# Performance work log

Hardware: AMD Instinct MI355X
Metric: run time of the kernel (lower is better)

Reference implementation:

```python
import jax, jax.numpy as jnp
import numpy as np

EMB = 384
H = 6
D = 64  # head_size = EMB // H
FF = 4 * EMB
B, T = 256, 256
EPS = 1e-5


def layernorm(x, g, b):
    mu = jnp.mean(x, axis=-1, keepdims=True)
    var = jnp.var(x, axis=-1, keepdims=True)
    return (x - mu) * jax.lax.rsqrt(var + EPS) * g + b


def setup_inputs() -> dict:
    key = jax.random.key(0)
    ks = jax.random.split(key, 12)
    s_qkv = 1.0 / np.sqrt(EMB)
    return {
        "x":  jax.random.normal(ks[0], (B, T, EMB), jnp.float32),
        # per-head Q/K/V projections stacked: [EMB, H, D]
        "Wq": jax.random.normal(ks[1], (EMB, H, D), jnp.float32) * s_qkv,
        "Wk": jax.random.normal(ks[2], (EMB, H, D), jnp.float32) * s_qkv,
        "Wv": jax.random.normal(ks[3], (EMB, H, D), jnp.float32) * s_qkv,
        "Wo": jax.random.normal(ks[4], (EMB, EMB), jnp.float32) * s_qkv,
        "bo": jnp.zeros((EMB,), jnp.float32),
        "W1": jax.random.normal(ks[5], (EMB, FF), jnp.float32) * s_qkv,
        "b1": jnp.zeros((FF,), jnp.float32),
        "W2": jax.random.normal(ks[6], (FF, EMB), jnp.float32) * (1.0 / np.sqrt(FF)),
        "b2": jnp.zeros((EMB,), jnp.float32),
        "g1": jnp.ones((EMB,), jnp.float32),
        "be1": jnp.zeros((EMB,), jnp.float32),
        "g2": jnp.ones((EMB,), jnp.float32),
        "be2": jnp.zeros((EMB,), jnp.float32),
    }


def reference(x, Wq, Wk, Wv, Wo, bo, W1, b1, W2, b2, g1, be1, g2, be2):
    # pre-LN attention (unmasked encoder block, dropout in eval mode = identity)
    h = layernorm(x, g1, be1)                      # [B,T,C]
    q = jnp.einsum('btc,chd->bhtd', h, Wq)
    k = jnp.einsum('btc,chd->bhtd', h, Wk)
    v = jnp.einsum('btc,chd->bhtd', h, Wv)
    scores = jnp.einsum('bhtd,bhsd->bhts', q, k) * (D ** -0.5)
    attn = jax.nn.softmax(scores, axis=-1)         # [B,H,T,T]
    o = jnp.einsum('bhts,bhsd->bhtd', attn, v)
    o = o.transpose(0, 2, 1, 3).reshape(x.shape[0], x.shape[1], EMB)  # concat heads
    x = x + o @ Wo + bo
    h2 = layernorm(x, g2, be2)
    ff = jax.nn.relu(h2 @ W1 + b1) @ W2 + b2
    return x + ff
```

## Files before the change

### kernel.cpp

```cpp
#include <hip/hip_runtime.h>

typedef __attribute__((ext_vector_type(8))) short bf16x8;
typedef __attribute__((ext_vector_type(4))) float f32x4;
typedef __attribute__((ext_vector_type(4))) unsigned short u16x4;
typedef __attribute__((ext_vector_type(4))) unsigned int u32x4;

#define DEVFN static __device__ __forceinline__

DEVFN unsigned short f2b(float f) {
  union { float f; unsigned u; } x; x.f = f;
  unsigned r = x.u + 0x7FFFu + ((x.u >> 16) & 1u);
  return (unsigned short)(r >> 16);
}

DEVFN unsigned cvtpk(float lo, float hi) {
  unsigned r;
  asm("v_cvt_pk_bf16_f32 %0, %1, %2" : "=v"(r) : "v"(lo), "v"(hi));
  return r;
}

DEVFN void gll16(const void* g, void* l) {
  __builtin_amdgcn_global_load_lds(
      (const __attribute__((address_space(1))) unsigned int*)g,
      (__attribute__((address_space(3))) unsigned int*)l, 16, 0, 0);
}

#define MFMA16(a, b, c) __builtin_amdgcn_mfma_f32_16x16x32_bf16((a), (b), (c), 0, 0, 0)

__global__ __launch_bounds__(256) void prep_kernel(
    const float* __restrict__ Wq, const float* __restrict__ Wk, const float* __restrict__ Wv,
    const float* __restrict__ Wo, const float* __restrict__ W1, const float* __restrict__ W2,
    short* __restrict__ wqkvT, short* __restrict__ woT,
    short* __restrict__ w1T, short* __restrict__ w2T)
{
  int idx = blockIdx.x * 256 + threadIdx.x;
  if (idx < 442368) {
    int n = idx / 384, kk = idx - n * 384;
    int sec = n / 384, ww = n - sec * 384;
    const float* s = sec == 0 ? Wq : (sec == 1 ? Wk : Wv);
    wqkvT[idx] = (short)f2b(s[kk * 384 + ww]);
  } else if (idx < 589824) {
    int j = idx - 442368;
    int n = j / 384, kk = j - n * 384;
    woT[j] = (short)f2b(Wo[kk * 384 + n]);
  } else if (idx < 1179648) {
    int j = idx - 589824;
    int n = j / 384, kk = j - n * 384;
    w1T[j] = (short)f2b(W1[kk * 1536 + n]);
  } else if (idx < 1769472) {
    int j = idx - 1179648;
    int n = j / 1536, kk = j - n * 1536;
    w2T[j] = (short)f2b(W2[kk * 384 + n]);
  }
}

__global__ __launch_bounds__(256) void ln_kernel(
    const float* __restrict__ x, const float* __restrict__ g, const float* __restrict__ b,
    short* __restrict__ out)
{
  int row = blockIdx.x * 4 + (threadIdx.x >> 6);
  int l = threadIdx.x & 63;
  const float* xr = x + (size_t)row * 384;
  float v[6], s = 0.f, s2 = 0.f;
  #pragma unroll
  for (int i = 0; i < 6; ++i) { v[i] = xr[l + 64 * i]; s += v[i]; s2 += v[i] * v[i]; }
  #pragma unroll
  for (int m = 1; m < 64; m <<= 1) { s += __shfl_xor(s, m); s2 += __shfl_xor(s2, m); }
  float mu = s * (1.f / 384.f);
  float rs = rsqrtf(s2 * (1.f / 384.f) - mu * mu + 1e-5f);
  short* orow = out + (size_t)row * 384;
  #pragma unroll
  for (int i = 0; i < 6; ++i) {
    int c = l + 64 * i;
    orow[c] = (short)f2b((v[i] - mu) * rs * g[c] + b[c]);
  }
}

template<int EPI>
__global__ __launch_bounds__(512) void gemm_bt(
    const short* __restrict__ A, const short* __restrict__ BT,
    int K, int kt, int N, int nx,
    const float* __restrict__ bias, const float* __restrict__ resid,
    float* __restrict__ fout, short* __restrict__ bout,
    short* __restrict__ qb, short* __restrict__ kb, short* __restrict__ vb)
{
  __shared__ short As[256 * 64];
  __shared__ short Bs[128 * 64];
  const int tid = threadIdx.x;
  const int l = tid & 63, w = tid >> 6;
  const int cl = l & 15, rq = l >> 4;
  const int wr = (w >> 1) * 64, wc = (w & 1) * 64;

  const int nwg = gridDim.x, bid = blockIdx.x;
  const int q8 = nwg >> 3, r8 = nwg & 7;
  const int xcd = bid & 7, ii = bid >> 3;
  const int wg = (xcd < r8) ? xcd * (q8 + 1) + ii : r8 * (q8 + 1) + (xcd - r8) * q8 + ii;
  const int bx = wg % nx, by = wg / nx;

  const int m0 = by * 256, n0 = bx * 128;
  const short* Ab = A + (size_t)m0 * K;
  const short* Bb = BT + (size_t)n0 * K;

  f32x4 acc[4][4] = {};

  for (int ks = 0; ks < kt; ++ks) {
    const int k0 = ks * 64;
    __syncthreads();
    #pragma unroll
    for (int i = 0; i < 4; ++i) {
      int slot = i * 512 + tid;
      int row = slot >> 3, g = slot & 7;
      int gs = g ^ (row & 7);
      gll16(Ab + (size_t)row * K + k0 + gs * 8, &As[slot * 8]);
    }
    #pragma unroll
    for (int i = 0; i < 2; ++i) {
      int slot = i * 512 + tid;
      int row = slot >> 3, g = slot & 7;
      int gs = g ^ (row & 7);
      gll16(Bb + (size_t)row * K + k0 + gs * 8, &Bs[slot * 8]);
    }
    __syncthreads();
    #pragma unroll
    for (int kk = 0; kk < 2; ++kk) {
      bf16x8 af[4], bfr[4];
      #pragma unroll
      for (int m = 0; m < 4; ++m) {
        int row = wr + m * 16 + cl;
        af[m] = *(const bf16x8*)&As[row * 64 + (((kk * 4 + rq) ^ (row & 7)) * 8)];
      }
      #pragma unroll
      for (int n = 0; n < 4; ++n) {
        int row = wc + n * 16 + cl;
        bfr[n] = *(const bf16x8*)&Bs[row * 64 + (((kk * 4 + rq) ^ (row & 7)) * 8)];
      }
      #pragma unroll
      for (int m = 0; m < 4; ++m)
        #pragma unroll
        for (int n = 0; n < 4; ++n)
          acc[m][n] = MFMA16(af[m], bfr[n], acc[m][n]);
    }
  }

  const int gr0 = m0 + wr, gc0 = n0 + wc;
  #pragma unroll
  for (int m = 0; m < 4; ++m) {
    #pragma unroll
    for (int n = 0; n < 4; ++n) {
      int col = gc0 + n * 16 + cl;
      int rbase = gr0 + m * 16 + rq * 4;
      if constexpr (EPI == 0) {
        int sec = col / 384;
        int wcol = col - sec * 384;
        int hh = wcol >> 6, d = wcol & 63;
        int bidx = rbase >> 8, t0 = rbase & 255;
        if (sec == 2) {
          u16x4 pk;
          #pragma unroll
          for (int r = 0; r < 4; ++r) pk[r] = f2b(acc[m][n][r]);
          *(u16x4*)&vb[((size_t)(bidx * 6 + hh) * 64 + d) * 256 + t0] = pk;
        } else {
          short* dst = (sec == 0) ? qb : kb;
          float sc = (sec == 0) ? 0.125f : 1.0f;
          #pragma unroll
          for (int r = 0; r < 4; ++r)
            dst[((size_t)(bidx * 6 + hh) * 256 + t0 + r) * 64 + d] = (short)f2b(acc[m][n][r] * sc);
        }
      } else if constexpr (EPI == 1) {
        #pragma unroll
        for (int r = 0; r < 4; ++r) {
          size_t ix = (size_t)(rbase + r) * N + col;
          fout[ix] = acc[m][n][r] + bias[col] + resid[ix];
        }
      } else {
        #pragma unroll
        for (int r = 0; r < 4; ++r)
          bout[(size_t)(rbase + r) * N + col] = (short)f2b(fmaxf(acc[m][n][r] + bias[col], 0.f));
      }
    }
  }
}

__global__ __launch_bounds__(1024) void attn_kernel(
    const short* __restrict__ qg, const short* __restrict__ kg,
    const short* __restrict__ vg, short* __restrict__ og)
{
  __shared__ short Ks[256 * 64];
  __shared__ short Vs[64 * 256];
  const int tid = threadIdx.x;
  const int bh = blockIdx.x;
  const int w = tid >> 6, l = tid & 63;
  const int cl = l & 15, rq = l >> 4;
  const short* kgb = kg + (size_t)bh * 16384;
  const short* vgb = vg + (size_t)bh * 16384;
  #pragma unroll
  for (int i = 0; i < 2; ++i) {
    int slot = i * 1024 + tid;
    int row = slot >> 3, g = slot & 7;
    gll16(kgb + row * 64 + (g ^ (row & 7)) * 8, &Ks[slot * 8]);
  }
  #pragma unroll
  for (int i = 0; i < 2; ++i) {
    int slot = i * 1024 + tid;
    int row = slot >> 5, g = slot & 31;
    int gs = (g & 24) | ((g ^ row) & 7);
    gll16(vgb + row * 256 + gs * 8, &Vs[slot * 8]);
  }
  const int qrow = w * 16 + cl;
  const bf16x8* qp = (const bf16x8*)(qg + ((size_t)bh * 256 + qrow) * 64 + rq * 8);
  bf16x8 qf0 = qp[0], qf1 = qp[4];
  const int b = bh / 6, hh = bh - b * 6;
  __syncthreads();

  f32x4 s[16] = {};
  #pragma unroll
  for (int c = 0; c < 16; ++c) {
    int srow = c * 16 + cl;
    bf16x8 k0 = *(const bf16x8*)&Ks[srow * 64 + ((rq ^ (srow & 7)) * 8)];
    bf16x8 k1 = *(const bf16x8*)&Ks[srow * 64 + (((4 + rq) ^ (srow & 7)) * 8)];
    s[c] = MFMA16(k0, qf0, s[c]);
    s[c] = MFMA16(k1, qf1, s[c]);
  }
  float mr[8];
  #pragma unroll
  for (int c = 0; c < 8; ++c)
    mr[c] = fmaxf(fmaxf(fmaxf(s[2*c][0], s[2*c][1]), fmaxf(s[2*c][2], s[2*c][3])),
                  fmaxf(fmaxf(s[2*c+1][0], s[2*c+1][1]), fmaxf(s[2*c+1][2], s[2*c+1][3])));
  float m = fmaxf(fmaxf(fmaxf(mr[0], mr[1]), fmaxf(mr[2], mr[3])),
                  fmaxf(fmaxf(mr[4], mr[5]), fmaxf(mr[6], mr[7])));
  m = fmaxf(m, __shfl_xor(m, 16));
  m = fmaxf(m, __shfl_xor(m, 32));
  float tc[16];
  #pragma unroll
  for (int c = 0; c < 16; ++c) {
    #pragma unroll
    for (int r = 0; r < 4; ++r) s[c][r] = __expf(s[c][r] - m);
    tc[c] = (s[c][0] + s[c][1]) + (s[c][2] + s[c][3]);
  }
  float t = ((tc[0]+tc[1])+(tc[2]+tc[3])) + ((tc[4]+tc[5])+(tc[6]+tc[7]))
          + ((tc[8]+tc[9])+(tc[10]+tc[11])) + ((tc[12]+tc[13])+(tc[14]+tc[15]));
  t += __shfl_xor(t, 16);
  t += __shfl_xor(t, 32);
  const float inv = 1.f / t;

  f32x4 oacc[4] = {};
  const int idx1 = (((2 * rq) & 3) * 16 + cl) << 2;
  const int idx2 = (((2 * rq + 1) & 3) * 16 + cl) << 2;
  const bool up = rq >= 2;
  #pragma unroll
  for (int ch = 0; ch < 8; ++ch) {
    int X0 = (int)cvtpk(s[2*ch][0], s[2*ch][1]);
    int X1 = (int)cvtpk(s[2*ch][2], s[2*ch][3]);
    int X2 = (int)cvtpk(s[2*ch+1][0], s[2*ch+1][1]);
    int X3 = (int)cvtpk(s[2*ch+1][2], s[2*ch+1][3]);
    int lo0 = __builtin_amdgcn_ds_bpermute(idx1, X0);
    int lo1 = __builtin_amdgcn_ds_bpermute(idx1, X1);
    int hi0 = __builtin_amdgcn_ds_bpermute(idx1, X2);
    int hi1 = __builtin_amdgcn_ds_bpermute(idx1, X3);
    int lo2 = __builtin_amdgcn_ds_bpermute(idx2, X0);
    int lo3 = __builtin_amdgcn_ds_bpermute(idx2, X1);
    int hi2 = __builtin_amdgcn_ds_bpermute(idx2, X2);
    int hi3 = __builtin_amdgcn_ds_bpermute(idx2, X3);
    u32x4 words;
    words[0] = (unsigned)(up ? hi0 : lo0);
    words[1] = (unsigned)(up ? hi1 : lo1);
    words[2] = (unsigned)(up ? hi2 : lo2);
    words[3] = (unsigned)(up ? hi3 : lo3);
    bf16x8 pa = __builtin_bit_cast(bf16x8, words);
    #pragma unroll
    for (int n = 0; n < 4; ++n) {
      int vrow = n * 16 + cl;
      int gg = ch * 4 + rq;
      int gs = (gg & 24) | ((gg ^ vrow) & 7);
      bf16x8 vf = *(const bf16x8*)&Vs[vrow * 256 + gs * 8];
      oacc[n] = MFMA16(pa, vf, oacc[n]);
    }
  }
  float invr[4];
  #pragma unroll
  for (int r = 0; r < 4; ++r) invr[r] = __shfl(inv, 4 * rq + r);
  #pragma unroll
  for (int n = 0; n < 4; ++n) {
    #pragma unroll
    for (int r = 0; r < 4; ++r) {
      int trow = w * 16 + 4 * rq + r;
      og[((size_t)(b * 256 + trow)) * 384 + hh * 64 + n * 16 + cl] =
          (short)f2b(oacc[n][r] * invr[r]);
    }
  }
}

extern "C" void kernel_launch(void* const* d_in, const int* in_sizes, int n_in,
                              void* d_out, int out_size, void* d_ws, size_t ws_size,
                              hipStream_t stream) {
  const float* x   = (const float*)d_in[0];
  const float* Wq  = (const float*)d_in[1];
  const float* Wk  = (const float*)d_in[2];
  const float* Wv  = (const float*)d_in[3];
  const float* Wo  = (const float*)d_in[4];
  const float* bo  = (const float*)d_in[5];
  const float* W1  = (const float*)d_in[6];
  const float* b1  = (const float*)d_in[7];
  const float* W2  = (const float*)d_in[8];
  const float* b2  = (const float*)d_in[9];
  const float* g1  = (const float*)d_in[10];
  const float* be1 = (const float*)d_in[11];
  const float* g2  = (const float*)d_in[12];
  const float* be2 = (const float*)d_in[13];

  char* ws = (char*)d_ws;
  short* wqkvT = (short*)(ws);
  short* woT   = (short*)(ws + 884736);
  short* w1T   = (short*)(ws + 1179648);
  short* w2T   = (short*)(ws + 2359296);
  short* bufA  = (short*)(ws + 3538944);
  short* h  = bufA;
  short* q  = bufA + 25165824;
  short* k  = bufA + 50331648;
  short* v  = bufA + 75497472;
  short* o  = bufA;
  short* h2 = bufA + 25165824;
  short* act = bufA + 50331648;
  float* out = (float*)d_out;

  prep_kernel<<<6912, 256, 0, stream>>>(Wq, Wk, Wv, Wo, W1, W2, wqkvT, woT, w1T, w2T);
  ln_kernel<<<16384, 256, 0, stream>>>(x, g1, be1, h);
  gemm_bt<0><<<9 * 256, 512, 0, stream>>>(h, wqkvT, 384, 6, 1152, 9,
      nullptr, nullptr, nullptr, nullptr, q, k, v);
  attn_kernel<<<1536, 1024, 0, stream>>>(q, k, v, o);
  gemm_bt<1><<<3 * 256, 512, 0, stream>>>(o, woT, 384, 6, 384, 3,
      bo, x, out, nullptr, nullptr, nullptr, nullptr);
  ln_kernel<<<16384, 256, 0, stream>>>(out, g2, be2, h2);
  for (int c = 0; c < 2; ++c) {
    const size_t roff = (size_t)c * 32768 * 384;
    const size_t ooff = (size_t)c * 32768 * 384;
    gemm_bt<2><<<12 * 128, 512, 0, stream>>>(h2 + roff, w1T, 384, 6, 1536, 12,
        b1, nullptr, nullptr, act, nullptr, nullptr, nullptr);
    gemm_bt<1><<<3 * 128, 512, 0, stream>>>(act, w2T, 1536, 24, 384, 3,
        b2, out + ooff, out + ooff, nullptr, nullptr, nullptr, nullptr);
  }
}
```

Baseline: 514.0 us.

## Fuse FFN up and down projections into one kernel keeping activations in LDS

Replaces the two-stage FFN (W1 GEMM writing bf16 activations to global memory, then W2 GEMM reading them back) with one fused kernel. Each block owns 128 rows and loops over 12 hidden-dim chunks, computing relu(h2·W1+b1) into shared memory and immediately accumulating into the 128x384 output. It also folds the 1/sqrt(D) Q scaling into the weight prep instead of the QKV epilogue. This removes the round trip of the large intermediate through HBM, but launches only 512 blocks with heavy LDS use, so occupancy is limited. The W1/W2 tile loads and MFMAs are not double-buffered and sit between barriers.

```diff
diff --git a/kernel.cpp b/kernel.cpp
--- a/kernel.cpp
+++ b/kernel.cpp
@@ -4,6 +4,7 @@
 typedef __attribute__((ext_vector_type(4))) float f32x4;
 typedef __attribute__((ext_vector_type(4))) unsigned short u16x4;
 typedef __attribute__((ext_vector_type(4))) unsigned int u32x4;
+typedef __attribute__((ext_vector_type(2))) unsigned int u32x2;
 
 #define DEVFN static __device__ __forceinline__
 
@@ -38,7 +39,8 @@
     int n = idx / 384, kk = idx - n * 384;
     int sec = n / 384, ww = n - sec * 384;
     const float* s = sec == 0 ? Wq : (sec == 1 ? Wk : Wv);
-    wqkvT[idx] = (short)f2b(s[kk * 384 + ww]);
+    float sc = (sec == 0) ? 0.125f : 1.0f;
+    wqkvT[idx] = (short)f2b(s[kk * 384 + ww] * sc);
   } else if (idx < 589824) {
     int j = idx - 442368;
     int n = j / 384, kk = j - n * 384;
@@ -81,7 +83,7 @@
     const short* __restrict__ A, const short* __restrict__ BT,
     int K, int kt, int N, int nx,
     const float* __restrict__ bias, const float* __restrict__ resid,
-    float* __restrict__ fout, short* __restrict__ bout,
+    float* __restrict__ fout,
     short* __restrict__ qb, short* __restrict__ kb, short* __restrict__ vb)
 {
   __shared__ short As[256 * 64];
@@ -161,21 +163,121 @@
           *(u16x4*)&vb[((size_t)(bidx * 6 + hh) * 64 + d) * 256 + t0] = pk;
         } else {
           short* dst = (sec == 0) ? qb : kb;
-          float sc = (sec == 0) ? 0.125f : 1.0f;
           #pragma unroll
           for (int r = 0; r < 4; ++r)
-            dst[((size_t)(bidx * 6 + hh) * 256 + t0 + r) * 64 + d] = (short)f2b(acc[m][n][r] * sc);
+            dst[((size_t)(bidx * 6 + hh) * 256 + t0 + r) * 64 + d] = (short)f2b(acc[m][n][r]);
         }
-      } else if constexpr (EPI == 1) {
+      } else {
         #pragma unroll
         for (int r = 0; r < 4; ++r) {
           size_t ix = (size_t)(rbase + r) * N + col;
           fout[ix] = acc[m][n][r] + bias[col] + resid[ix];
         }
-      } else {
-        #pragma unroll
-        for (int r = 0; r < 4; ++r)
-          bout[(size_t)(rbase + r) * N + col] = (short)f2b(fmaxf(acc[m][n][r] + bias[col], 0.f));
+      }
+    }
+  }
+}
+
+__global__ __launch_bounds__(512, 2) void ff_fused(
+    const short* __restrict__ h2,
+    const short* __restrict__ w1T,
+    const short* __restrict__ w2T,
+    const float* __restrict__ b1, const float* __restrict__ b2,
+    float* __restrict__ out)
+{
+  __shared__ short As[128 * 64];
+  __shared__ short W1s[128 * 64];
+  __shared__ short Acts[128 * 128];
+  __shared__ short W2s[384 * 64];
+  const int tid = threadIdx.x;
+  const int l = tid & 63, w = tid >> 6;
+  const int cl = l & 15, rq = l >> 4;
+  const int wm = w >> 2, wn = w & 3;
+  const int m0 = blockIdx.x * 128;
+
+  f32x4 acc[4][6] = {};
+
+  for (int c = 0; c < 12; ++c) {
+    f32x4 aacc[8] = {};
+    for (int ks = 0; ks < 6; ++ks) {
+      __syncthreads();
+      #pragma unroll
+      for (int i = 0; i < 2; ++i) {
+        int slot = i * 512 + tid;
+        int row = slot >> 3, g = slot & 7;
+        int gs = g ^ (row & 7);
+        gll16(h2 + (size_t)(m0 + row) * 384 + ks * 64 + gs * 8, &As[slot * 8]);
+        gll16(w1T + (size_t)(c * 128 + row) * 384 + ks * 64 + gs * 8, &W1s[slot * 8]);
+      }
+      __syncthreads();
+      #pragma unroll
+      for (int kk = 0; kk < 2; ++kk) {
+        int wrow = w * 16 + cl;
+        bf16x8 w1f = *(const bf16x8*)&W1s[wrow * 64 + (((kk * 4 + rq) ^ (wrow & 7)) * 8)];
+        #pragma unroll
+        for (int m8 = 0; m8 < 8; ++m8) {
+          int arow = m8 * 16 + cl;
+          bf16x8 hf = *(const bf16x8*)&As[arow * 64 + (((kk * 4 + rq) ^ (arow & 7)) * 8)];
+          aacc[m8] = MFMA16(w1f, hf, aacc[m8]);
+        }
+      }
+    }
+    f32x4 b1v = *(const f32x4*)&b1[c * 128 + w * 16 + 4 * rq];
+    #pragma unroll
+    for (int m8 = 0; m8 < 8; ++m8) {
+      int row = m8 * 16 + cl;
+      int gran = 2 * w + (rq >> 1);
+      int off = row * 128 + ((gran ^ (row & 7)) * 8) + ((rq & 1) * 4);
+      float v0 = fmaxf(aacc[m8][0] + b1v[0], 0.f);
+      float v1 = fmaxf(aacc[m8][1] + b1v[1], 0.f);
+      float v2 = fmaxf(aacc[m8][2] + b1v[2], 0.f);
+      float v3 = fmaxf(aacc[m8][3] + b1v[3], 0.f);
+      u32x2 pw; pw[0] = cvtpk(v0, v1); pw[1] = cvtpk(v2, v3);
+      *(u32x2*)&Acts[off] = pw;
+    }
+    #pragma unroll
+    for (int fk = 0; fk < 2; ++fk) {
+      __syncthreads();
+      #pragma unroll
+      for (int i = 0; i < 6; ++i) {
+        int slot = i * 512 + tid;
+        int row = slot >> 3, g = slot & 7;
+        int gs = g ^ (row & 7);
+        gll16(w2T + (size_t)row * 1536 + c * 128 + fk * 64 + gs * 8, &W2s[slot * 8]);
+      }
+      __syncthreads();
+      #pragma unroll
+      for (int kk = 0; kk < 2; ++kk) {
+        bf16x8 af[4], bf[6];
+        #pragma unroll
+        for (int m = 0; m < 4; ++m) {
+          int row = wm * 64 + m * 16 + cl;
+          int gran = fk * 8 + kk * 4 + rq;
+          af[m] = *(const bf16x8*)&Acts[row * 128 + ((gran ^ (row & 7)) * 8)];
+        }
+        #pragma unroll
+        for (int n = 0; n < 6; ++n) {
+          int row = wn * 96 + n * 16 + cl;
+          bf[n] = *(const bf16x8*)&W2s[row * 64 + (((kk * 4 + rq) ^ (row & 7)) * 8)];
+        }
+        #pragma unroll
+        for (int m = 0; m < 4; ++m)
+          #pragma unroll
+          for (int n = 0; n < 6; ++n)
+            acc[m][n] = MFMA16(af[m], bf[n], acc[m][n]);
+      }
+    }
+  }
+  #pragma unroll
+  for (int m = 0; m < 4; ++m) {
+    #pragma unroll
+    for (int n = 0; n < 6; ++n) {
+      int col = wn * 96 + n * 16 + cl;
+      int rbase = m0 + wm * 64 + m * 16 + 4 * rq;
+      #pragma unroll
+      for (int r = 0; r < 4; ++r) {
+        size_t ix = (size_t)(rbase + r) * 384 + col;
+        out[ix] = acc[m][n][r] + b2[col] + out[ix];
       }
     }
   }
@@ -320,23 +422,15 @@
   short* v  = bufA + 75497472;
   short* o  = bufA;
   short* h2 = bufA + 25165824;
-  short* act = bufA + 50331648;
   float* out = (float*)d_out;
 
   prep_kernel<<<6912, 256, 0, stream>>>(Wq, Wk, Wv, Wo, W1, W2, wqkvT, woT, w1T, w2T);
   ln_kernel<<<16384, 256, 0, stream>>>(x, g1, be1, h);
   gemm_bt<0><<<9 * 256, 512, 0, stream>>>(h, wqkvT, 384, 6, 1152, 9,
-      nullptr, nullptr, nullptr, nullptr, q, k, v);
+      nullptr, nullptr, nullptr, q, k, v);
   attn_kernel<<<1536, 1024, 0, stream>>>(q, k, v, o);
   gemm_bt<1><<<3 * 256, 512, 0, stream>>>(o, woT, 384, 6, 384, 3,
-      bo, x, out, nullptr, nullptr, nullptr, nullptr);
+      bo, x, out, nullptr, nullptr, nullptr);
   ln_kernel<<<16384, 256, 0, stream>>>(out, g2, be2, h2);
-  for (int c = 0; c < 2; ++c) {
-    const size_t roff = (size_t)c * 32768 * 384;
-    const size_t ooff = (size_t)c * 32768 * 384;
-    gemm_bt<2><<<12 * 128, 512, 0, stream>>>(h2 + roff, w1T, 384, 6, 1536, 12,
-        b1, nullptr, nullptr, act, nullptr, nullptr, nullptr);
-    gemm_bt<1><<<3 * 128, 512, 0, stream>>>(act, w2T, 1536, 24, 384, 3,
-        b2, out + ooff, out + ooff, nullptr, nullptr, nullptr, nullptr);
-  }
-}
+  ff_fused<<<512, 512, 0, stream>>>(h2, w1T, w2T, b1, b2, out);
+}
```

Measured after the change: 583.5 us. 13.5% more time.
